# Performance work log

Hardware: AMD Instinct MI355X
Metric: run time of the kernel (lower is better)

The kernel has to match this reference:

```python
import jax, jax.numpy as jnp
import numpy as np

EPS = 1e-5
NEG_SLOPE = 0.2

def _linear(x, w, b):
    return x @ w.T + b

def _seg_softmax(a, dst, n):
    # numerically stable softmax over edges grouped by destination node
    m = jax.ops.segment_max(a, dst, num_segments=n)
    e = jnp.exp(a - m[dst])
    s = jax.ops.segment_sum(e, dst, num_segments=n)
    return e / (s[dst] + 1e-16)

def _gat(x, src, dst, n, w, a_src, a_dst, b):
    # PyG GATConv, heads=1: h = xW^T; alpha = LeakyReLU(a_s.h_src + a_d.h_dst)
    h = x @ w.T                                   # [N,H]
    al_s = (h * a_src).sum(-1)                    # [N]
    al_d = (h * a_dst).sum(-1)                    # [N]
    alpha = jax.nn.leaky_relu(al_s[src] + al_d[dst], NEG_SLOPE)  # [E]
    attn = _seg_softmax(alpha, dst, n)
    out = jax.ops.segment_sum(attn[:, None] * h[src], dst, num_segments=n)
    return out + b

def _bn(x, g, b):
    # BatchNorm over the node dimension (training-style batch stats, eval dropout)
    mu = x.mean(0)
    var = x.var(0)
    return (x - mu) * jax.lax.rsqrt(var + EPS) * g + b

def setup_inputs() -> dict:
    key = jax.random.key(0)
    N, E, SAT, NEI, H, OUT = 50000, 1600000, 32, 32, 128, 16
    ks = jax.random.split(key, 26)
    p = lambda k, shape, s=0.05: jax.random.normal(k, shape, jnp.float32) * s
    return {
        "x": jax.random.normal(ks[0], (N, SAT + NEI), jnp.float32),
        "edge_index": jax.random.randint(ks[1], (2, E), 0, N, jnp.int32),
        "sat_w": p(ks[2], (H, SAT)), "sat_b": jnp.zeros((H,), jnp.float32),
        "neigh_w": p(ks[3], (H, NEI)), "neigh_b": jnp.zeros((H,), jnp.float32),
        "fus_w": p(ks[4], (1, 2 * H)), "fus_b": jnp.zeros((1,), jnp.float32),
        "w1": p(ks[5], (H, H)), "as1": p(ks[6], (H,)), "ad1": p(ks[7], (H,)), "b1": jnp.zeros((H,), jnp.float32),
        "g1": jnp.ones((H,), jnp.float32), "be1": jnp.zeros((H,), jnp.float32),
        "w2": p(ks[8], (H, H)), "as2": p(ks[9], (H,)), "ad2": p(ks[10], (H,)), "b2": jnp.zeros((H,), jnp.float32),
        "g2": jnp.ones((H,), jnp.float32), "be2": jnp.zeros((H,), jnp.float32),
        "fc1_w": p(ks[11], (H, H)), "fc1_b": jnp.zeros((H,), jnp.float32),
        "fc2_w": p(ks[12], (OUT, H)), "fc2_b": jnp.zeros((OUT,), jnp.float32),
    }

def reference(x, edge_index, sat_w, sat_b, neigh_w, neigh_b, fus_w, fus_b,
              w1, as1, ad1, b1, g1, be1, w2, as2, ad2, b2, g2, be2,
              fc1_w, fc1_b, fc2_w, fc2_b):
    n = x.shape[0]
    sat_dim = sat_w.shape[1]
    sat = jax.nn.relu(_linear(x[:, :sat_dim], sat_w, sat_b))
    nei = jax.nn.relu(_linear(x[:, sat_dim:], neigh_w, neigh_b))
    gate = jax.nn.sigmoid(_linear(jnp.concatenate([sat, nei], axis=1), fus_w, fus_b))
    h = gate * sat + (1.0 - gate) * nei
    # GATConv adds self-loops by default
    loops = jnp.arange(n, dtype=edge_index.dtype)
    src = jnp.concatenate([edge_index[0], loops])
    dst = jnp.concatenate([edge_index[1], loops])
    res = h
    h = jax.nn.relu(_bn(_gat(h, src, dst, n, w1, as1, ad1, b1), g1, be1)) + res
    res = h
    h = jax.nn.relu(_bn(_gat(h, src, dst, n, w2, as2, ad2, b2), g2, be2)) + res
    h = jax.nn.relu(_linear(h, fc1_w, fc1_b))
    return _linear(h, fc2_w, fc2_b)
```

## Files before the change

### kernel.cpp

```cpp
#include <hip/hip_runtime.h>

#define H 128

typedef __attribute__((ext_vector_type(8))) short bf16x8;
typedef __attribute__((ext_vector_type(4))) float f32x4;

__device__ __forceinline__ float bf2f(unsigned short u) {
    return __uint_as_float(((unsigned)u) << 16);
}
__device__ __forceinline__ unsigned short f2bf(float f) {
    unsigned u = __float_as_uint(f);
    unsigned r = (u + 0x7fffu + ((u >> 16) & 1u)) >> 16;
    return (unsigned short)r;
}
__device__ __forceinline__ unsigned pack2bf(float a, float b) {
    return (unsigned)f2bf(a) | ((unsigned)f2bf(b) << 16);
}

__global__ void fuse_kernel(const float* __restrict__ x,
                            const float* __restrict__ sat_w, const float* __restrict__ sat_b,
                            const float* __restrict__ neigh_w, const float* __restrict__ neigh_b,
                            const float* __restrict__ fus_w, const float* __restrict__ fus_b,
                            unsigned short* __restrict__ h0b,
                            float* __restrict__ accum, int* __restrict__ bukTot, int N) {
    __shared__ unsigned smem[8512];
    __shared__ float reds[4][64];
    unsigned* a_lds = smem;
    unsigned* w_lds = smem + 2304;
    int tid = threadIdx.x;
    int base = blockIdx.x * 64;
    if (blockIdx.x == 0) {
        for (int i = tid; i < 4096; i += 256) accum[i] = 0.f;
        bukTot[tid] = 0;
    }
    for (int i = tid; i < 64 * 32; i += 256) {
        int n = i >> 5, kp = i & 31;
        int gn = base + n;
        float2 v = (gn < N) ? *(const float2*)(x + (size_t)gn * 64 + kp * 2) : make_float2(0.f, 0.f);
        a_lds[n * 36 + kp] = pack2bf(v.x, v.y);
    }
    for (int i = tid; i < 256 * 16; i += 256) {
        int r = i >> 4, kp = i & 15;
        const float* wsrc = (r < 128) ? (sat_w + (size_t)r * 32) : (neigh_w + (size_t)(r - 128) * 32);
        float2 v = *(const float2*)(wsrc + kp * 2);
        w_lds[r * 20 + kp] = pack2bf(v.x, v.y);
    }
    __syncthreads();
    int lane = tid & 63;
    int wv = tid >> 6;
    int lr = lane & 15, lk = lane >> 4;
    f32x4 accS[4][2], accN[4][2];
#pragma unroll
    for (int r = 0; r < 4; ++r)
#pragma unroll
        for (int t = 0; t < 2; ++t) {
            accS[r][t] = (f32x4){0.f, 0.f, 0.f, 0.f};
            accN[r][t] = (f32x4){0.f, 0.f, 0.f, 0.f};
        }
    bf16x8 afS[4], afN[4];
#pragma unroll
    for (int r = 0; r < 4; ++r) {
        afS[r] = *(const bf16x8*)&a_lds[(r * 16 + lr) * 36 + lk * 4];
        afN[r] = *(const bf16x8*)&a_lds[(r * 16 + lr) * 36 + 16 + lk * 4];
    }
#pragma unroll
    for (int t = 0; t < 2; ++t) {
        bf16x8 bS = *(const bf16x8*)&w_lds[(wv * 32 + t * 16 + lr) * 20 + lk * 4];
        bf16x8 bN = *(const bf16x8*)&w_lds[(128 + wv * 32 + t * 16 + lr) * 20 + lk * 4];
#pragma unroll
        for (int r = 0; r < 4; ++r) {
            accS[r][t] = __builtin_amdgcn_mfma_f32_16x16x32_bf16(afS[r], bS, accS[r][t], 0, 0, 0);
            accN[r][t] = __builtin_amdgcn_mfma_f32_16x16x32_bf16(afN[r], bN, accN[r][t], 0, 0, 0);
        }
    }
    __syncthreads();
    unsigned short* cst = (unsigned short*)smem;
#pragma unroll
    for (int t = 0; t < 2; ++t) {
        int col = wv * 32 + t * 16 + lr;
        float sb = sat_b[col], nb = neigh_b[col];
#pragma unroll
        for (int r = 0; r < 4; ++r) {
#pragma unroll
            for (int j = 0; j < 4; ++j) {
                int srow = r * 16 + lk * 4 + j;
                cst[srow * 266 + col] = f2bf(fmaxf(accS[r][t][j] + sb, 0.f));
                cst[srow * 266 + 133 + col] = f2bf(fmaxf(accN[r][t][j] + nb, 0.f));
            }
        }
    }
    __syncthreads();
    int node = tid & 63;
    int part = tid >> 6;
    float ps = 0.f;
#pragma unroll
    for (int k = 0; k < 32; ++k) {
        int col = part * 32 + k;
        ps += bf2f(cst[node * 266 + col]) * fus_w[col]
            + bf2f(cst[node * 266 + 133 + col]) * fus_w[128 + col];
    }
    reds[part][node] = ps;
    __syncthreads();
    float tot = reds[0][node] + reds[1][node] + reds[2][node] + reds[3][node];
    float g = 1.f / (1.f + __expf(-(tot + fus_b[0])));
    if (base + node < N) {
        unsigned* op = (unsigned*)h0b + (size_t)(base + node) * 64 + part * 16;
#pragma unroll
        for (int kp = 0; kp < 16; ++kp) {
            int col = part * 32 + kp * 2;
            float o0 = g * bf2f(cst[node * 266 + col]) + (1.f - g) * bf2f(cst[node * 266 + 133 + col]);
            float o1 = g * bf2f(cst[node * 266 + col + 1]) + (1.f - g) * bf2f(cst[node * 266 + 134 + col]);
            op[kp] = pack2bf(o0, o1);
        }
    }
}

template <int TAG, int MODE>
__global__ void gemm128m(const void* __restrict__ inv, const float* __restrict__ w,
                         const float* __restrict__ bias, int do_relu,
                         unsigned short* __restrict__ outb, int N,
                         const float* __restrict__ a_sp, const float* __restrict__ a_dp,
                         float* __restrict__ al_s, float* __restrict__ al_d,
                         const float* __restrict__ accum8, const float* __restrict__ gvec,
                         const float* __restrict__ bevec,
                         const unsigned short* __restrict__ resb, unsigned* __restrict__ yout) {
    __shared__ unsigned a_lds[64 * 68];
    __shared__ unsigned w_lds[128 * 68];
    __shared__ float reds[4][64];
    __shared__ float redd[4][64];
    __shared__ float sc_l[128], sh_l[128];
    int tid = threadIdx.x;
    int base = blockIdx.x * 64;
    if (MODE == 2) {
        if (tid < 128) {
            float s = 0.f, q = 0.f;
#pragma unroll
            for (int c = 0; c < 8; ++c) {
                s += accum8[c * 256 + tid];
                q += accum8[c * 256 + 128 + tid];
            }
            float Ninv = 1.f / (float)N;
            float mu = s * Ninv;
            float var = q * Ninv - mu * mu;
            float sc = rsqrtf(var + 1e-5f) * gvec[tid];
            sc_l[tid] = sc;
            sh_l[tid] = bevec[tid] - mu * sc;
        }
        __syncthreads();
    }
    for (int i = tid; i < 64 * 64; i += 256) {
        int n = i >> 6, kp = i & 63;
        int gn = base + n;
        unsigned p = 0u;
        if (gn < N) {
            if (MODE == 1) {
                p = ((const unsigned*)inv)[(size_t)gn * 64 + kp];
            } else {
                float2 v = *(const float2*)((const float*)inv + (size_t)gn * 128 + kp * 2);
                float2 sc = ((const float2*)sc_l)[kp];
                float2 sh = ((const float2*)sh_l)[kp];
                ushort2 rr = ((const ushort2*)(resb + (size_t)gn * 128))[kp];
                float y0 = fmaxf(v.x * sc.x + sh.x, 0.f) + bf2f(rr.x);
                float y1 = fmaxf(v.y * sc.y + sh.y, 0.f) + bf2f(rr.y);
                p = pack2bf(y0, y1);
                if (yout) yout[(size_t)gn * 64 + kp] = p;
            }
        }
        a_lds[n * 68 + kp] = p;
    }
    for (int i = tid; i < 128 * 64; i += 256) {
        int c = i >> 6, kp = i & 63;
        float2 v = *(const float2*)(w + (size_t)c * 128 + kp * 2);
        w_lds[c * 68 + kp] = pack2bf(v.x, v.y);
    }
    __syncthreads();
    int lane = tid & 63;
    int wv = tid >> 6;
    int lr = lane & 15;
    int lk = lane >> 4;
    f32x4 acc[4][2];
#pragma unroll
    for (int r = 0; r < 4; ++r)
#pragma unroll
        for (int t = 0; t < 2; ++t) acc[r][t] = (f32x4){0.f, 0.f, 0.f, 0.f};
    for (int c = 0; c < 4; ++c) {
        bf16x8 af[4], bfr[2];
#pragma unroll
        for (int r = 0; r < 4; ++r)
            af[r] = *(const bf16x8*)&a_lds[(r * 16 + lr) * 68 + c * 16 + lk * 4];
#pragma unroll
        for (int t = 0; t < 2; ++t)
            bfr[t] = *(const bf16x8*)&w_lds[(wv * 32 + t * 16 + lr) * 68 + c * 16 + lk * 4];
#pragma unroll
        for (int r = 0; r < 4; ++r)
#pragma unroll
            for (int t = 0; t < 2; ++t)
                acc[r][t] = __builtin_amdgcn_mfma_f32_16x16x32_bf16(af[r], bfr[t], acc[r][t], 0, 0, 0);
    }
    __syncthreads();
    unsigned short* cst = (unsigned short*)a_lds;
#pragma unroll
    for (int t = 0; t < 2; ++t) {
        int col = wv * 32 + t * 16 + lr;
        float bv = bias ? bias[col] : 0.f;
#pragma unroll
        for (int r = 0; r < 4; ++r) {
#pragma unroll
            for (int j = 0; j < 4; ++j) {
                float v = acc[r][t][j] + bv;
                if (do_relu) v = fmaxf(v, 0.f);
                cst[(r * 16 + lk * 4 + j) * 136 + col] = f2bf(v);
            }
        }
    }
    __syncthreads();
    for (int i = tid; i < 64 * 64; i += 256) {
        int n = i >> 6, kp = i & 63;
        int gn = base + n;
        if (gn < N) ((unsigned*)outb)[(size_t)gn * 64 + kp] = a_lds[n * 68 + kp];
    }
    if (a_sp) {
        int node = tid & 63;
        int part = tid >> 6;
        float ps = 0.f, pd = 0.f;
        int kb = part * 32;
        const unsigned short* xr = cst + node * 136 + kb;
#pragma unroll
        for (int k = 0; k < 32; ++k) {
            float v = bf2f(xr[k]);
            ps += v * a_sp[kb + k];
            pd += v * a_dp[kb + k];
        }
        reds[part][node] = ps;
        redd[part][node] = pd;
        __syncthreads();
        if (tid < 64) {
            int gn = base + tid;
            if (gn < N) {
                al_s[gn] = reds[0][tid] + reds[1][tid] + reds[2][tid] + reds[3][tid];
                al_d[gn] = redd[0][tid] + redd[1][tid] + redd[2][tid] + redd[3][tid];
            }
        }
    }
}

#define PBMAX 6400
#define NBSTR 256
__global__ void pack_bucket(const int* __restrict__ src, const int* __restrict__ dst,
                            unsigned* __restrict__ pk2, int* __restrict__ cntBB,
                            int* __restrict__ offBB, int* __restrict__ bukTot, int E, int PB) {
    __shared__ unsigned opk[PBMAX];
    __shared__ unsigned opk2[PBMAX];
    __shared__ int lcnt[256];
    __shared__ int tmp[256];
    int tid = threadIdx.x;
    int blk = blockIdx.x;
    int e0 = blk * PB;
    int n = min(PB, E - e0);
    if (n < 0) n = 0;
    lcnt[tid] = 0;
    __syncthreads();
    for (int i = tid; i < n; i += 256) {
        int s = src[e0 + i];
        int d = dst[e0 + i];
        unsigned p = ((unsigned)d << 16) | (unsigned)s;
        opk[i] = p;
        atomicAdd(&lcnt[d >> 8], 1);
    }
    __syncthreads();
    int v = lcnt[tid];
    tmp[tid] = v;
    __syncthreads();
    for (int off = 1; off < 256; off <<= 1) {
        int u = (tid >= off) ? tmp[tid - off] : 0;
        __syncthreads();
        tmp[tid] += u;
        __syncthreads();
    }
    int excl = tmp[tid] - v;
    cntBB[(size_t)tid * NBSTR + blk] = v;
    offBB[(size_t)tid * NBSTR + blk] = excl;
    if (v > 0) atomicAdd(&bukTot[tid], v);
    lcnt[tid] = excl;
    __syncthreads();
    for (int i = tid; i < n; i += 256) {
        unsigned p = opk[i];
        int pos = atomicAdd(&lcnt[(p >> 16) >> 8], 1);
        opk2[pos] = p;
    }
    __syncthreads();
    for (int i = tid; i < n; i += 256) pk2[e0 + i] = opk2[i];
}

#define BCAP 10240
__global__ void scatter_sort2(const unsigned* __restrict__ pk2, const int* __restrict__ cntBB,
                              const int* __restrict__ offBB, const int* __restrict__ bukTot,
                              int* __restrict__ ssrc, int* __restrict__ rowptr,
                              int N, int E, int PB) {
    __shared__ int segoff[257];
    __shared__ int segsrc[256];
    __shared__ int segcnt[256];
    __shared__ int lcur[256];
    __shared__ int tmp[256];
    __shared__ int bt[256];
    __shared__ int gb_sh;
    __shared__ unsigned opk[BCAP];
    __shared__ int osrc[BCAP];
    int b = blockIdx.x;
    int d0 = b << 8;
    int tid = threadIdx.x;
    int btv = bukTot[tid];
    bt[tid] = btv;
    tmp[tid] = btv;
    __syncthreads();
    for (int off = 1; off < 256; off <<= 1) {
        int u = (tid >= off) ? tmp[tid - off] : 0;
        __syncthreads();
        tmp[tid] += u;
        __syncthreads();
    }
    if (tid == 0) {
        gb_sh = tmp[b] - bt[b];
        if (b == 0) rowptr[N] = E;
    }
    __syncthreads();
    int c = cntBB[(size_t)b * NBSTR + tid];
    segcnt[tid] = c;
    segsrc[tid] = tid * PB + offBB[(size_t)b * NBSTR + tid];
    tmp[tid] = c;
    lcur[tid] = 0;
    __syncthreads();
    for (int off = 1; off < 256; off <<= 1) {
        int u = (tid >= off) ? tmp[tid - off] : 0;
        __syncthreads();
        tmp[tid] += u;
        __syncthreads();
    }
    segoff[tid] = tmp[tid] - segcnt[tid];
    if (tid == 255) segoff[256] = tmp[255];
    __syncthreads();
    int cntb = segoff[256];
    int wv = tid >> 6, lane = tid & 63;
    for (int s = wv; s < 256; s += 4) {
        int sc = segcnt[s], so = segoff[s], gs = segsrc[s];
        for (int i = lane; i < sc; i += 64) opk[so + i] = pk2[gs + i];
    }
    __syncthreads();
    for (int i = tid; i < cntb; i += 256)
        atomicAdd(&lcur[(opk[i] >> 16) & 255], 1);
    __syncthreads();
    int v = lcur[tid];
    tmp[tid] = v;
    __syncthreads();
    for (int off = 1; off < 256; off <<= 1) {
        int u = (tid >= off) ? tmp[tid - off] : 0;
        __syncthreads();
        tmp[tid] += u;
        __syncthreads();
    }
    int excl = tmp[tid] - v;
    int gbase = gb_sh;
    if (d0 + tid < N) rowptr[d0 + tid] = gbase + excl;
    lcur[tid] = excl;
    __syncthreads();
    for (int i = tid; i < cntb; i += 256) {
        unsigned p = opk[i];
        int pos = atomicAdd(&lcur[(p >> 16) & 255], 1);
        osrc[pos] = (int)(p & 0xFFFFu);
    }
    __syncthreads();
    for (int i = tid; i < cntb; i += 256) ssrc[gbase + i] = osrc[i];
}

template <int TAG>
__global__ void gat_agg(const int* __restrict__ rowptr, const int* __restrict__ ssrc,
                        const float* __restrict__ al_s, const float* __restrict__ al_d,
                        const unsigned short* __restrict__ hb, float* __restrict__ out,
                        float* __restrict__ accum8, int N) {
    __shared__ int s_sv[4][64];
    __shared__ float s_ev[4][64];
    __shared__ float ys[4][128];
    __shared__ float yq[4][128];
    int tid = threadIdx.x;
    int wiw = tid >> 6;
    int w = (blockIdx.x * blockDim.x + tid) >> 6;
    int lane = tid & 63;
    int sub = lane >> 5;
    int fl = lane & 31;
    float a0 = 0.f, a1 = 0.f, a2 = 0.f, a3 = 0.f;
    float ss = 0.f;
    if (w < N) {
        int beg = rowptr[w], end = rowptr[w + 1];
        float ald = al_d[w];
        float a_self = al_s[w] + ald;
        a_self = (a_self > 0.f) ? a_self : 0.2f * a_self;
        float m = a_self;
        for (int e = beg + lane; e < end; e += 64) {
            float a = al_s[ssrc[e]] + ald;
            a = (a > 0.f) ? a : 0.2f * a;
            m = fmaxf(m, a);
        }
        for (int off = 32; off; off >>= 1) m = fmaxf(m, __shfl_xor(m, off));
        for (int base = beg; base < end; base += 64) {
            int nch = min(64, end - base);
            int sv = 0;
            float ev = 0.f;
            if (lane < nch) {
                sv = ssrc[base + lane];
                float a = al_s[sv] + ald;
                a = (a > 0.f) ? a : 0.2f * a;
                ev = __expf(a - m);
            }
            ss += ev;
            s_sv[wiw][lane] = sv;
            s_ev[wiw][lane] = ev;
            for (int j0 = 0; j0 < nch; j0 += 8) {
                ushort4 hv[4];
                float evv[4];
#pragma unroll
                for (int jj = 0; jj < 4; ++jj) {
                    int j = j0 + 2 * jj + sub;
                    bool ok = j < nch;
                    int svj = ok ? s_sv[wiw][j] : 0;
                    evv[jj] = ok ? s_ev[wiw][j] : 0.f;
                    hv[jj] = ((const ushort4*)(hb + (size_t)svj * H))[fl];
                }
#pragma unroll
                for (int jj = 0; jj < 4; ++jj) {
                    a0 += evv[jj] * bf2f(hv[jj].x);
                    a1 += evv[jj] * bf2f(hv[jj].y);
                    a2 += evv[jj] * bf2f(hv[jj].z);
                    a3 += evv[jj] * bf2f(hv[jj].w);
                }
            }
        }
        for (int off = 32; off; off >>= 1) ss += __shfl_xor(ss, off);
        a0 += __shfl_xor(a0, 32);
        a1 += __shfl_xor(a1, 32);
        a2 += __shfl_xor(a2, 32);
        a3 += __shfl_xor(a3, 32);
        float ev_self = __expf(a_self - m);
        ss += ev_self;
        ushort4 hs = ((const ushort4*)(hb + (size_t)w * H))[fl];
        a0 += ev_self * bf2f(hs.x);
        a1 += ev_self * bf2f(hs.y);
        a2 += ev_self * bf2f(hs.z);
        a3 += ev_self * bf2f(hs.w);
        float inv = 1.f / (ss + 1e-16f);
        a0 *= inv; a1 *= inv; a2 *= inv; a3 *= inv;
        if (sub == 0) {
            ((float4*)(out + (size_t)w * H))[fl] = make_float4(a0, a1, a2, a3);
        }
    }
    if (sub == 0) {
        float4 yy = (w < N) ? make_float4(a0, a1, a2, a3) : make_float4(0.f, 0.f, 0.f, 0.f);
        ((float4*)&ys[wiw][0])[fl] = yy;
        ((float4*)&yq[wiw][0])[fl] = make_float4(yy.x * yy.x, yy.y * yy.y, yy.z * yy.z, yy.w * yy.w);
    }
    __syncthreads();
    if (tid < 128) {
        float s = ys[0][tid] + ys[1][tid] + ys[2][tid] + ys[3][tid];
        float q = yq[0][tid] + yq[1][tid] + yq[2][tid] + yq[3][tid];
        float* ac = accum8 + (size_t)(blockIdx.x & 7) * 256;
        atomicAdd(ac + tid, s);
        atomicAdd(ac + 128 + tid, q);
    }
}

__global__ void fc2_kernel(const unsigned short* __restrict__ in, const float* __restrict__ w,
                           const float* __restrict__ b, float* __restrict__ out,
                           int N, int OUT) {
    __shared__ float wsm[16 * 132];
    __shared__ float xs[16][129];
    int tid = threadIdx.x;
    for (int i = tid; i < OUT * H; i += 256) {
        int o = i >> 7, k = i & 127;
        wsm[o * 132 + k] = w[i];
    }
    int nb = blockIdx.x * 16;
    for (int i = tid; i < 16 * 128; i += 256) {
        int n = i >> 7, k = i & 127;
        int gn = nb + n;
        xs[n][k] = (gn < N) ? bf2f(in[(size_t)gn * H + k]) : 0.f;
    }
    __syncthreads();
    int o = tid & 15;
    int nn = tid >> 4;
    int n = nb + nn;
    if (n >= N || o >= OUT) return;
    const float* xr = xs[nn];
    const float* wr = wsm + o * 132;
    float acc = b[o];
#pragma unroll 8
    for (int k = 0; k < H; k += 4) {
        acc += xr[k] * wr[k] + xr[k + 1] * wr[k + 1] + xr[k + 2] * wr[k + 2] + xr[k + 3] * wr[k + 3];
    }
    out[(size_t)n * OUT + o] = acc;
}


extern "C" void kernel_launch(void* const* d_in, const int* in_sizes, int n_in,
                              void* d_out, int out_size, void* d_ws, size_t ws_size,
                              hipStream_t stream) {
    const float* x       = (const float*)d_in[0];
    const int*   ei      = (const int*)d_in[1];
    const float* sat_w   = (const float*)d_in[2];
    const float* sat_b   = (const float*)d_in[3];
    const float* neigh_w = (const float*)d_in[4];
    const float* neigh_b = (const float*)d_in[5];
    const float* fus_w   = (const float*)d_in[6];
    const float* fus_b   = (const float*)d_in[7];
    const float* w1      = (const float*)d_in[8];
    const float* as1     = (const float*)d_in[9];
    const float* ad1     = (const float*)d_in[10];
    const float* g1      = (const float*)d_in[12];
    const float* be1     = (const float*)d_in[13];
    const float* w2      = (const float*)d_in[14];
    const float* as2     = (const float*)d_in[15];
    const float* ad2     = (const float*)d_in[16];
    const float* g2      = (const float*)d_in[18];
    const float* be2     = (const float*)d_in[19];
    const float* fc1_w   = (const float*)d_in[20];
    const float* fc1_b   = (const float*)d_in[21];
    const float* fc2_w   = (const float*)d_in[22];
    const float* fc2_b   = (const float*)d_in[23];

    int N = in_sizes[0] / 64;
    int E = in_sizes[1] / 2;
    int OUT = in_sizes[23];
    int PB = (E + 255) / 256;
    int NBUKET = (N + 255) >> 8;

    float* ws    = (float*)d_ws;
    float* h0    = ws;
    float* hA    = h0 + (size_t)N * H;
    float* agg   = hA + (size_t)N * H;
    float* al_s  = agg + (size_t)N * H;
    float* al_d  = al_s + N;
    float* accum = al_d + N;
    int* rowptr  = (int*)(accum + 4096);
    int* cntBB   = rowptr + (N + 1);
    int* offBB   = cntBB + 256 * NBSTR;
    int* bukTot  = offBB + 256 * NBSTR;
    int* ssrc    = bukTot + 256;
    unsigned* pk2= (unsigned*)(ssrc + E);
    unsigned* y1b= pk2 + E;
    unsigned short* hAb = (unsigned short*)hA;
    unsigned short* h0b = (unsigned short*)(hA + (size_t)N * 64);

    const int* srcp = ei;
    const int* dstp = ei + E;

    dim3 b256(256);
    int gGemm = (N + 63) / 64;
    int gWaveN = (N + 3) / 4;

    fuse_kernel<<<gGemm, b256, 0, stream>>>(x, sat_w, sat_b, neigh_w, neigh_b, fus_w, fus_b,
                                            h0b, accum, bukTot, N);

    pack_bucket<<<256, b256, 0, stream>>>(srcp, dstp, pk2, cntBB, offBB, bukTot, E, PB);
    scatter_sort2<<<NBUKET, b256, 0, stream>>>(pk2, cntBB, offBB, bukTot, ssrc, rowptr, N, E, PB);

    gemm128m<1, 1><<<gGemm, b256, 0, stream>>>(h0b, w1, nullptr, 0, hAb, N, as1, ad1, al_s, al_d,
                                               nullptr, nullptr, nullptr, nullptr, nullptr);
    gat_agg<1><<<gWaveN, b256, 0, stream>>>(rowptr, ssrc, al_s, al_d, hAb, agg, accum, N);

    gemm128m<2, 2><<<gGemm, b256, 0, stream>>>(agg, w2, nullptr, 0, hAb, N, as2, ad2, al_s, al_d,
                                               accum, g1, be1, h0b, y1b);
    gat_agg<2><<<gWaveN, b256, 0, stream>>>(rowptr, ssrc, al_s, al_d, hAb, h0, accum + 2048, N);

    gemm128m<3, 2><<<gGemm, b256, 0, stream>>>(h0, fc1_w, fc1_b, 1, hAb, N, nullptr, nullptr,
                                               nullptr, nullptr, accum + 2048, g2, be2,
                                               (const unsigned short*)y1b, nullptr);
    fc2_kernel<<<(N + 15) / 16, b256, 0, stream>>>(hAb, fc2_w, fc2_b, (float*)d_out, N, OUT);
}
```

Before: 299.2 us.

## Split GAT aggregation into softmax-prep and column-sliced gather kernels

Replaces the single per-node GAT aggregation kernel with two kernels. The first computes the edge logits once with an online max and sum, then stores the logits, the max, the inverse denominator and the self-loop weight. The second gathers neighbor features with four blocks per node, each handling a 32-column slice, so more waves are in flight. This removes the double logit pass and raises parallelism for the gather. In exchange it adds an extra launch, a write and read of per-edge logits, and reads ssrc and rowptr four times.

```diff
diff --git a/kernel.cpp b/kernel.cpp
--- a/kernel.cpp
+++ b/kernel.cpp
@@ -373,97 +373,113 @@
 }
 
 template <int TAG>
-__global__ void gat_agg(const int* __restrict__ rowptr, const int* __restrict__ ssrc,
-                        const float* __restrict__ al_s, const float* __restrict__ al_d,
-                        const unsigned short* __restrict__ hb, float* __restrict__ out,
-                        float* __restrict__ accum8, int N) {
+__global__ void attn_prep(const int* __restrict__ rowptr, const int* __restrict__ ssrc,
+                          const float* __restrict__ al_s, const float* __restrict__ al_d,
+                          float* __restrict__ alog, float* __restrict__ mArr,
+                          float* __restrict__ invArr, float* __restrict__ evsArr, int N) {
+    int w = (blockIdx.x * blockDim.x + threadIdx.x) >> 6;
+    int lane = threadIdx.x & 63;
+    if (w >= N) return;
+    int beg = rowptr[w], end = rowptr[w + 1];
+    float ald = al_d[w];
+    float m_l = -1e30f, ss_l = 0.f;
+    for (int e = beg + lane; e < end; e += 64) {
+        float a = al_s[ssrc[e]] + ald;
+        a = (a > 0.f) ? a : 0.2f * a;
+        alog[e] = a;
+        float Mn = fmaxf(m_l, a);
+        ss_l = ss_l * __expf(m_l - Mn) + __expf(a - Mn);
+        m_l = Mn;
+    }
+    for (int off = 32; off; off >>= 1) {
+        float m_o = __shfl_xor(m_l, off);
+        float s_o = __shfl_xor(ss_l, off);
+        float Mn = fmaxf(m_l, m_o);
+        ss_l = ss_l * __expf(m_l - Mn) + s_o * __expf(m_o - Mn);
+        m_l = Mn;
+    }
+    float a_self = al_s[w] + ald;
+    a_self = (a_self > 0.f) ? a_self : 0.2f * a_self;
+    float M2 = fmaxf(m_l, a_self);
+    float ss = ss_l * __expf(m_l - M2) + __expf(a_self - M2);
+    if (lane == 0) {
+        mArr[w] = M2;
+        invArr[w] = 1.f / (ss + 1e-16f);
+        evsArr[w] = __expf(a_self - M2);
+    }
+}
+
+template <int TAG>
+__global__ void gat_gather(const int* __restrict__ rowptr, const int* __restrict__ ssrc,
+                           const float* __restrict__ alog, const float* __restrict__ mArr,
+                           const float* __restrict__ invArr, const float* __restrict__ evsArr,
+                           const unsigned short* __restrict__ hb, float* __restrict__ out,
+                           float* __restrict__ accum8, int N) {
     __shared__ int s_sv[4][64];
-    __shared__ float s_ev[4][64];
-    __shared__ float ys[4][128];
-    __shared__ float yq[4][128];
+    __shared__ float s_at[4][64];
+    __shared__ float ys[4][32];
+    __shared__ float yq[4][32];
     int tid = threadIdx.x;
     int wiw = tid >> 6;
-    int w = (blockIdx.x * blockDim.x + tid) >> 6;
     int lane = tid & 63;
-    int sub = lane >> 5;
-    int fl = lane & 31;
-    float a0 = 0.f, a1 = 0.f, a2 = 0.f, a3 = 0.f;
-    float ss = 0.f;
+    int c = blockIdx.x & 3;
+    int w = (blockIdx.x >> 2) * 4 + wiw;
+    int sub = lane >> 4;
+    int fl = lane & 15;
+    float acc0 = 0.f, acc1 = 0.f;
+    float y0 = 0.f, y1 = 0.f;
     if (w < N) {
         int beg = rowptr[w], end = rowptr[w + 1];
-        float ald = al_d[w];
-        float a_self = al_s[w] + ald;
-        a_self = (a_self > 0.f) ? a_self : 0.2f * a_self;
-        float m = a_self;
-        for (int e = beg + lane; e < end; e += 64) {
-            float a = al_s[ssrc[e]] + ald;
-            a = (a > 0.f) ? a : 0.2f * a;
-            m = fmaxf(m, a);
-        }
-        for (int off = 32; off; off >>= 1) m = fmaxf(m, __shfl_xor(m, off));
+        float Mw = mArr[w];
         for (int base = beg; base < end; base += 64) {
             int nch = min(64, end - base);
-            int sv = 0;
-            float ev = 0.f;
             if (lane < nch) {
-                sv = ssrc[base + lane];
-                float a = al_s[sv] + ald;
-                a = (a > 0.f) ? a : 0.2f * a;
-                ev = __expf(a - m);
+                s_sv[wiw][lane] = ssrc[base + lane];
+                s_at[wiw][lane] = __expf(alog[base + lane] - Mw);
             }
-            ss += ev;
-            s_sv[wiw][lane] = sv;
-            s_ev[wiw][lane] = ev;
-            for (int j0 = 0; j0 < nch; j0 += 8) {
-                ushort4 hv[4];
-                float evv[4];
+            for (int j0 = 0; j0 < nch; j0 += 16) {
+                ushort2 hv[4];
+                float av[4];
 #pragma unroll
                 for (int jj = 0; jj < 4; ++jj) {
-                    int j = j0 + 2 * jj + sub;
+                    int j = j0 + 4 * jj + sub;
                     bool ok = j < nch;
-                    int svj = ok ? s_sv[wiw][j] : 0;
-                    evv[jj] = ok ? s_ev[wiw][j] : 0.f;
-                    hv[jj] = ((const ushort4*)(hb + (size_t)svj * H))[fl];
+                    int sv = ok ? s_sv[wiw][j] : 0;
+                    av[jj] = ok ? s_at[wiw][j] : 0.f;
+                    hv[jj] = ((const ushort2*)(hb + (size_t)sv * H))[c * 16 + fl];
                 }
 #pragma unroll
                 for (int jj = 0; jj < 4; ++jj) {
-                    a0 += evv[jj] * bf2f(hv[jj].x);
-                    a1 += evv[jj] * bf2f(hv[jj].y);
-                    a2 += evv[jj] * bf2f(hv[jj].z);
-                    a3 += evv[jj] * bf2f(hv[jj].w);
+                    acc0 += av[jj] * bf2f(hv[jj].x);
+                    acc1 += av[jj] * bf2f(hv[jj].y);
                 }
             }
         }
-        for (int off = 32; off; off >>= 1) ss += __shfl_xor(ss, off);
-        a0 += __shfl_xor(a0, 32);
-        a1 += __shfl_xor(a1, 32);
-        a2 += __shfl_xor(a2, 32);
-        a3 += __shfl_xor(a3, 32);
-        float ev_self = __expf(a_self - m);
-        ss += ev_self;
-        ushort4 hs = ((const ushort4*)(hb + (size_t)w * H))[fl];
-        a0 += ev_self * bf2f(hs.x);
-        a1 += ev_self * bf2f(hs.y);
-        a2 += ev_self * bf2f(hs.z);
-        a3 += ev_self * bf2f(hs.w);
-        float inv = 1.f / (ss + 1e-16f);
-        a0 *= inv; a1 *= inv; a2 *= inv; a3 *= inv;
+        acc0 += __shfl_xor(acc0, 16);
+        acc0 += __shfl_xor(acc0, 32);
+        acc1 += __shfl_xor(acc1, 16);
+        acc1 += __shfl_xor(acc1, 32);
         if (sub == 0) {
-            ((float4*)(out + (size_t)w * H))[fl] = make_float4(a0, a1, a2, a3);
+            float evs = evsArr[w], inv = invArr[w];
+            ushort2 hs = ((const ushort2*)(hb + (size_t)w * H))[c * 16 + fl];
+            y0 = (acc0 + evs * bf2f(hs.x)) * inv;
+            y1 = (acc1 + evs * bf2f(hs.y)) * inv;
+            ((float2*)(out + (size_t)w * H))[c * 16 + fl] = make_float2(y0, y1);
         }
     }
     if (sub == 0) {
-        float4 yy = (w < N) ? make_float4(a0, a1, a2, a3) : make_float4(0.f, 0.f, 0.f, 0.f);
-        ((float4*)&ys[wiw][0])[fl] = yy;
-        ((float4*)&yq[wiw][0])[fl] = make_float4(yy.x * yy.x, yy.y * yy.y, yy.z * yy.z, yy.w * yy.w);
-    }
-    __syncthreads();
-    if (tid < 128) {
+        ys[wiw][fl * 2] = y0;
+        ys[wiw][fl * 2 + 1] = y1;
+        yq[wiw][fl * 2] = y0 * y0;
+        yq[wiw][fl * 2 + 1] = y1 * y1;
+    }
+    __syncthreads();
+    if (tid < 32) {
         float s = ys[0][tid] + ys[1][tid] + ys[2][tid] + ys[3][tid];
         float q = yq[0][tid] + yq[1][tid] + yq[2][tid] + yq[3][tid];
         float* ac = accum8 + (size_t)(blockIdx.x & 7) * 256;
-        atomicAdd(ac + tid, s);
-        atomicAdd(ac + 128 + tid, q);
+        atomicAdd(ac + c * 32 + tid, s);
+        atomicAdd(ac + 128 + c * 32 + tid, q);
     }
 }
 
@@ -537,14 +553,18 @@
     float* agg   = hA + (size_t)N * H;
     float* al_s  = agg + (size_t)N * H;
     float* al_d  = al_s + N;
-    float* accum = al_d + N;
+    float* mArr  = al_d + N;
+    float* invAr = mArr + N;
+    float* evsAr = invAr + N;
+    float* accum = evsAr + N;
     int* rowptr  = (int*)(accum + 4096);
     int* cntBB   = rowptr + (N + 1);
     int* offBB   = cntBB + 256 * NBSTR;
     int* bukTot  = offBB + 256 * NBSTR;
     int* ssrc    = bukTot + 256;
     unsigned* pk2= (unsigned*)(ssrc + E);
-    unsigned* y1b= pk2 + E;
+    float* alog  = (float*)(pk2 + E);
+    unsigned* y1b= (unsigned*)(alog + E);
     unsigned short* hAb = (unsigned short*)hA;
     unsigned short* h0b = (unsigned short*)(hA + (size_t)N * 64);
 
@@ -563,11 +583,15 @@
 
     gemm128m<1, 1><<<gGemm, b256, 0, stream>>>(h0b, w1, nullptr, 0, hAb, N, as1, ad1, al_s, al_d,
                                                nullptr, nullptr, nullptr, nullptr, nullptr);
-    gat_agg<1><<<gWaveN, b256, 0, stream>>>(rowptr, ssrc, al_s, al_d, hAb, agg, accum, N);
+    attn_prep<1><<<gWaveN, b256, 0, stream>>>(rowptr, ssrc, al_s, al_d, alog, mArr, invAr, evsAr, N);
+    gat_gather<1><<<gWaveN * 4, b256, 0, stream>>>(rowptr, ssrc, alog, mArr, invAr, evsAr,
+                                                   hAb, agg, accum, N);
 
     gemm128m<2, 2><<<gGemm, b256, 0, stream>>>(agg, w2, nullptr, 0, hAb, N, as2, ad2, al_s, al_d,
                                                accum, g1, be1, h0b, y1b);
-    gat_agg<2><<<gWaveN, b256, 0, stream>>>(rowptr, ssrc, al_s, al_d, hAb, h0, accum + 2048, N);
+    attn_prep<2><<<gWaveN, b256, 0, stream>>>(rowptr, ssrc, al_s, al_d, alog, mArr, invAr, evsAr, N);
+    gat_gather<2><<<gWaveN * 4, b256, 0, stream>>>(rowptr, ssrc, alog, mArr, invAr, evsAr,
+                                                   hAb, h0, accum + 2048, N);
 
     gemm128m<3, 2><<<gGemm, b256, 0, stream>>>(h0, fc1_w, fc1_b, 1, hAb, N, nullptr, nullptr,
                                                nullptr, nullptr, accum + 2048, g2, be2,
```

After: 456.1 us. 52.4% more time.
